# Performance work log

Hardware: AMD Instinct MI355X
Metric: run time of the kernel (lower is better)

The kernel has to match this reference:

```python
import jax, jax.numpy as jnp
import numpy as np

N = 50000   # nodes
E = 800000  # edges
H = 3       # attention heads
IN_F = 128
HID = 128
NUM_CLASSES = 6
GAT_SLOPE = 0.2   # DGL GATConv internal leaky_relu slope
ACT_SLOPE = 0.01  # nn.LeakyReLU default


def setup_inputs() -> dict:
    key = jax.random.key(0)
    ks = jax.random.split(key, 24)
    s = 0.05
    inp = {
        "in_feat": jax.random.normal(ks[0], (N, IN_F), jnp.float32),
        "src": jax.random.randint(ks[1], (E,), 0, N, jnp.int32),
        "dst": jax.random.randint(ks[2], (E,), 0, N, jnp.int32),
        # GATConv 1: W (IN_F, H*HID), attn vectors (H, HID), bias (H*HID)
        "W1": jax.random.normal(ks[3], (IN_F, H * HID), jnp.float32) * s,
        "al1": jax.random.normal(ks[4], (H, HID), jnp.float32) * s,
        "ar1": jax.random.normal(ks[5], (H, HID), jnp.float32) * s,
        "b1": jnp.zeros((H * HID,), jnp.float32),
        # GATConv 2
        "W2": jax.random.normal(ks[6], (HID, H * HID), jnp.float32) * s,
        "al2": jax.random.normal(ks[7], (H, HID), jnp.float32) * s,
        "ar2": jax.random.normal(ks[8], (H, HID), jnp.float32) * s,
        "b2": jnp.zeros((H * HID,), jnp.float32),
    }
    # Dense MLP head lin1..lin4 (HID->HID) and lin5 (HID->NUM_CLASSES)
    for i in range(1, 5):
        inp[f"lw{i}"] = jax.random.normal(ks[8 + 2 * i], (HID, HID), jnp.float32) * s
        inp[f"lb{i}"] = jnp.zeros((HID,), jnp.float32)
    inp["lw5"] = jax.random.normal(ks[20], (HID, NUM_CLASSES), jnp.float32) * s
    inp["lb5"] = jnp.zeros((NUM_CLASSES,), jnp.float32)
    return inp


def gat_conv(x, src, dst, W, al, ar, b):
    # x: (N, F_in) -> out: (N, H, HID)
    h = (x @ W).reshape(N, H, HID)
    el = jnp.einsum('nhf,hf->nh', h, al)  # (N, H)
    er = jnp.einsum('nhf,hf->nh', h, ar)
    e = jax.nn.leaky_relu(el[src] + er[dst], GAT_SLOPE)  # (E, H)
    # edge softmax over incoming edges of each dst node
    m = jax.ops.segment_max(e, dst, num_segments=N)
    m = jnp.where(jnp.isfinite(m), m, 0.0)
    ex = jnp.exp(e - m[dst])
    denom = jax.ops.segment_sum(ex, dst, num_segments=N)
    alpha = ex / (denom[dst] + 1e-9)  # (E, H)
    out = jax.ops.segment_sum(alpha[:, :, None] * h[src], dst, num_segments=N)
    return out + b.reshape(1, H, HID)


def reference(in_feat, src, dst, W1, al1, ar1, b1, W2, al2, ar2, b2,
              lw1, lb1, lw2, lb2, lw3, lb3, lw4, lb4, lw5, lb5):
    act = lambda x: jax.nn.leaky_relu(x, ACT_SLOPE)
    h = act(gat_conv(in_feat, src, dst, W1, al1, ar1, b1)).mean(axis=1)
    h = act(gat_conv(h, src, dst, W2, al2, ar2, b2)).mean(axis=1)
    h = act(h @ lw1 + lb1)
    h = act(h @ lw2 + lb2)
    h = act(h @ lw3 + lb3)
    h = act(h @ lw4 + lb4)
    return h @ lw5 + lb5
```

## Files before the change

### kernel.cpp

```cpp
#include <hip/hip_runtime.h>
#include <hip/hip_bf16.h>


typedef __attribute__((ext_vector_type(8))) short short8;
typedef __attribute__((ext_vector_type(4))) float float4v;

__device__ inline short f2bf(float x) {
    union { float f; unsigned u; } v; v.f = x;
    unsigned r = v.u + 0x7FFFu + ((v.u >> 16) & 1u);
    return (short)(r >> 16);
}
__device__ inline float bf2f(short b) {
    union { float f; unsigned u; } v;
    v.u = ((unsigned)(unsigned short)b) << 16;
    return v.f;
}
__device__ inline short8 zero8() { short8 z = {0,0,0,0,0,0,0,0}; return z; }

__device__ __forceinline__ void gl_lds16(const short* g, short* l) {
    __builtin_amdgcn_global_load_lds(
        (const __attribute__((address_space(1))) void*)g,
        (__attribute__((address_space(3))) void*)l,
        16, 0, 0);
}

#define SW(r) ((((r) >> 2) ^ (r)) & 3)

#define BM 128
#define BN 128
#define BK 32
#define MSTR 136
#define MROWS 64

__global__ void prep_kernel(
    const float* __restrict__ in_feat, short* __restrict__ P1h,
    short* __restrict__ P1l, int n4, int cb, int wb,
    const int* __restrict__ dst, int* __restrict__ cnt, int E,
    const float* __restrict__ w1, const float* __restrict__ w2,
    const float* __restrict__ m1, const float* __restrict__ m2,
    const float* __restrict__ m3, const float* __restrict__ m4,
    const float* __restrict__ w5,
    short* __restrict__ w1h, short* __restrict__ w1l,
    short* __restrict__ w2h, short* __restrict__ w2l,
    short* __restrict__ m1h, short* __restrict__ m1l,
    short* __restrict__ m2h, short* __restrict__ m2l,
    short* __restrict__ m3h, short* __restrict__ m3l,
    short* __restrict__ m4h, short* __restrict__ m4l,
    short* __restrict__ w5h, short* __restrict__ w5l)
{
    int blk = blockIdx.x;
    if (blk < cb) {
        int i = blk * 256 + threadIdx.x;
        if (i >= n4) return;
        float4 v = *(const float4*)(in_feat + (size_t)i * 4);
        float xs[4] = {v.x, v.y, v.z, v.w};
        short hs[4], ls[4];
        #pragma unroll
        for (int j = 0; j < 4; ++j) {
            hs[j] = f2bf(xs[j]);
            ls[j] = f2bf(xs[j] - bf2f(hs[j]));
        }
        *(uint2*)(P1h + (size_t)i * 4) = *(uint2*)hs;
        *(uint2*)(P1l + (size_t)i * 4) = *(uint2*)ls;
    } else if (blk < cb + wb) {
        int j = (blk - cb) * 256 + threadIdx.x;
        const float* src; short* th; short* tl; int Nc, base;
        if      (j < 49152)  { src = w1; th = w1h; tl = w1l; Nc = 384; base = 0; }
        else if (j < 98304)  { src = w2; th = w2h; tl = w2l; Nc = 384; base = 49152; }
        else if (j < 114688) { src = m1; th = m1h; tl = m1l; Nc = 128; base = 98304; }
        else if (j < 131072) { src = m2; th = m2h; tl = m2l; Nc = 128; base = 114688; }
        else if (j < 147456) { src = m3; th = m3h; tl = m3l; Nc = 128; base = 131072; }
        else if (j < 163840) { src = m4; th = m4h; tl = m4l; Nc = 128; base = 147456; }
        else if (j < 164608) { src = w5; th = w5h; tl = w5l; Nc = 6;   base = 163840; }
        else return;
        int i = j - base;
        int k = i / Nc, c = i - k * Nc;
        float v = src[i];
        short h = f2bf(v);
        th[(size_t)c * 128 + k] = h;
        tl[(size_t)c * 128 + k] = f2bf(v - bf2f(h));
    } else {
        int e = (blk - cb - wb) * 256 + threadIdx.x;
        if (e < E) atomicAdd(&cnt[dst[e]], 1);
    }
}

__global__ __launch_bounds__(256) void gemm_mfma(
    const short* __restrict__ Ahi, const short* __restrict__ Alo,
    const short* __restrict__ Bth, const short* __restrict__ Btl,
    unsigned char* __restrict__ Cq,
    float* __restrict__ els, float* __restrict__ er,
    const float* __restrict__ al, const float* __restrict__ ar,
    int M, int Nc)
{
    __shared__ short Ah[BM * BK], Al_[BM * BK];
    __shared__ short Bh[BN * BK], Bl_[BN * BK];

    int tid = threadIdx.x, lane = tid & 63, wave = tid >> 6;
    int l15 = lane & 15, q = lane >> 4;
    int rowBase = blockIdx.y * BM, colBase = blockIdx.x * BN;

    float4v acc[2][8];
    #pragma unroll
    for (int mt = 0; mt < 2; ++mt)
        #pragma unroll
        for (int nt = 0; nt < 8; ++nt)
            acc[mt][nt] = (float4v){0.f, 0.f, 0.f, 0.f};

    for (int k0 = 0; k0 < 128; k0 += BK) {
        #pragma unroll
        for (int i = 0; i < 2; ++i) {
            int cid = tid + i * 256;
            int r = cid >> 2, sub = cid & 3;
            int gs = (sub ^ SW(r)) * 8;
            size_t ga = (size_t)(rowBase + r) * 128 + k0 + gs;
            size_t gb = (size_t)(colBase + r) * 128 + k0 + gs;
            int ld = cid * 8;
            gl_lds16(Ahi + ga, Ah  + ld);
            gl_lds16(Alo + ga, Al_ + ld);
            gl_lds16(Bth + gb, Bh  + ld);
            gl_lds16(Btl + gb, Bl_ + ld);
        }
        __syncthreads();

        short8 aH[2], aL2[2];
        #pragma unroll
        for (int mt = 0; mt < 2; ++mt) {
            int row = wave * 32 + mt * 16 + l15;
            int off = row * 32 + (q ^ SW(row)) * 8;
            aH[mt]  = *(short8*)&Ah[off];
            aL2[mt] = *(short8*)&Al_[off];
        }
        #pragma unroll
        for (int nt = 0; nt < 8; ++nt) {
            int row = nt * 16 + l15;
            int off = row * 32 + (q ^ SW(row)) * 8;
            short8 bH = *(short8*)&Bh[off];
            short8 bL = *(short8*)&Bl_[off];
            #pragma unroll
            for (int mt = 0; mt < 2; ++mt) {
                acc[mt][nt] = __builtin_amdgcn_mfma_f32_16x16x32_bf16(aH[mt], bH, acc[mt][nt], 0, 0, 0);
                acc[mt][nt] = __builtin_amdgcn_mfma_f32_16x16x32_bf16(aH[mt], bL, acc[mt][nt], 0, 0, 0);
                acc[mt][nt] = __builtin_amdgcn_mfma_f32_16x16x32_bf16(aL2[mt], bH, acc[mt][nt], 0, 0, 0);
            }
        }
        __syncthreads();
    }

    {
        const float* alh = al + colBase;
        const float* arh = ar + colBase;
        float pel[2][4] = {}, per_[2][4] = {};
        #pragma unroll
        for (int nt = 0; nt < 8; ++nt) {
            float av = alh[nt * 16 + l15];
            float rv = arh[nt * 16 + l15];
            #pragma unroll
            for (int mt = 0; mt < 2; ++mt)
                #pragma unroll
                for (int i = 0; i < 4; ++i) {
                    pel[mt][i]  += acc[mt][nt][i] * av;
                    per_[mt][i] += acc[mt][nt][i] * rv;
                }
        }
        #pragma unroll
        for (int mask = 1; mask < 16; mask <<= 1)
            #pragma unroll
            for (int mt = 0; mt < 2; ++mt)
                #pragma unroll
                for (int i = 0; i < 4; ++i) {
                    pel[mt][i]  += __shfl_xor(pel[mt][i], mask);
                    per_[mt][i] += __shfl_xor(per_[mt][i], mask);
                }
        if (l15 == 0) {
            #pragma unroll
            for (int mt = 0; mt < 2; ++mt)
                #pragma unroll
                for (int i = 0; i < 4; ++i) {
                    int r = rowBase + wave * 32 + mt * 16 + q * 4 + i;
                    if (r < M) {
                        els[(size_t)(r * 3 + blockIdx.x) * 2] = pel[mt][i];
                        er[r * 3 + blockIdx.x] = per_[mt][i];
                    }
                }
        }
    }

    #pragma unroll
    for (int mt = 0; mt < 2; ++mt) {
        #pragma unroll
        for (int i = 0; i < 4; ++i) {
            float rm = 0.f;
            #pragma unroll
            for (int nt = 0; nt < 8; ++nt)
                rm = fmaxf(rm, fabsf(acc[mt][nt][i]));
            #pragma unroll
            for (int mask = 1; mask < 16; mask <<= 1)
                rm = fmaxf(rm, __shfl_xor(rm, mask));
            int r = rowBase + wave * 32 + mt * 16 + q * 4 + i;
            float inv = 127.f / fmaxf(rm, 1e-30f);
            if (l15 == 0 && r < M)
                els[(size_t)(r * 3 + blockIdx.x) * 2 + 1] = rm * (1.f / 127.f);
            #pragma unroll
            for (int nt = 0; nt < 8; ++nt) {
                int c = colBase + nt * 16 + l15;
                int qi = (int)rintf(acc[mt][nt][i] * inv);
                int qn = __shfl_xor(qi, 1);
                if (!(l15 & 1) && r < M && c < Nc) {
                    unsigned short pk = (unsigned short)((qi & 0xFF) | ((qn & 0xFF) << 8));
                    *(unsigned short*)(Cq + (size_t)r * Nc + c) = pk;
                }
            }
        }
    }
}

__global__ __launch_bounds__(256) void mlp_fused(
    const short* __restrict__ Ph, const short* __restrict__ Pl,
    const short* __restrict__ w1h, const short* __restrict__ w1l,
    const short* __restrict__ w2h, const short* __restrict__ w2l,
    const short* __restrict__ w3h, const short* __restrict__ w3l,
    const short* __restrict__ w4h, const short* __restrict__ w4l,
    const short* __restrict__ w5h, const short* __restrict__ w5l,
    const float* __restrict__ b1, const float* __restrict__ b2,
    const float* __restrict__ b3, const float* __restrict__ b4,
    const float* __restrict__ b5,
    float* __restrict__ out, int M)
{
    __shared__ short AH[MROWS * MSTR], AL[MROWS * MSTR];
    __shared__ short WH[128 * BK], WL[128 * BK];

    int tid = threadIdx.x, lane = tid & 63, wave = tid >> 6;
    int l15 = lane & 15, q = lane >> 4;
    int rowBase = blockIdx.x * MROWS;

    #pragma unroll
    for (int s = 0; s < 4; ++s) {
        int idx = tid + s * 256;
        int r = idx >> 4, kq = (idx & 15) * 8;
        int gr = rowBase + r;
        short8 vh = zero8(), vl = zero8();
        if (gr < M) {
            vh = *(const short8*)(Ph + (size_t)gr * 128 + kq);
            vl = *(const short8*)(Pl + (size_t)gr * 128 + kq);
        }
        *(short8*)&AH[r * MSTR + kq] = vh;
        *(short8*)&AL[r * MSTR + kq] = vl;
    }

    const short* Whs[4] = {w1h, w2h, w3h, w4h};
    const short* Wls[4] = {w1l, w2l, w3l, w4l};
    const float* Bss[4] = {b1, b2, b3, b4};

    #pragma unroll
    for (int L = 0; L < 4; ++L) {
        float4v acc[8];
        #pragma unroll
        for (int nt = 0; nt < 8; ++nt)
            acc[nt] = (float4v){0.f, 0.f, 0.f, 0.f};

        for (int k0 = 0; k0 < 128; k0 += BK) {
            #pragma unroll
            for (int i = 0; i < 4; ++i) {
                int c2 = tid + (i & 1) * 256;
                int r = c2 >> 2, sub = c2 & 3;
                int gs = (sub ^ SW(r)) * 8;
                if (i < 2) gl_lds16(Whs[L] + (size_t)r * 128 + k0 + gs, WH + c2 * 8);
                else       gl_lds16(Wls[L] + (size_t)r * 128 + k0 + gs, WL + c2 * 8);
            }
            __syncthreads();
            int offa = (wave * 16 + l15) * MSTR + k0 + q * 8;
            short8 aH  = *(short8*)&AH[offa];
            short8 aL2 = *(short8*)&AL[offa];
            #pragma unroll
            for (int nt = 0; nt < 8; ++nt) {
                int row = nt * 16 + l15;
                int off = row * 32 + (q ^ SW(row)) * 8;
                short8 bH = *(short8*)&WH[off];
                short8 bL = *(short8*)&WL[off];
                acc[nt] = __builtin_amdgcn_mfma_f32_16x16x32_bf16(aH, bH, acc[nt], 0, 0, 0);
                acc[nt] = __builtin_amdgcn_mfma_f32_16x16x32_bf16(aH, bL, acc[nt], 0, 0, 0);
                acc[nt] = __builtin_amdgcn_mfma_f32_16x16x32_bf16(aL2, bH, acc[nt], 0, 0, 0);
            }
            __syncthreads();
        }
        #pragma unroll
        for (int nt = 0; nt < 8; ++nt) {
            int c = nt * 16 + l15;
            float bv = Bss[L][c];
            #pragma unroll
            for (int i = 0; i < 4; ++i) {
                int r = wave * 16 + q * 4 + i;
                float v = acc[nt][i] + bv;
                v = (v < 0.f) ? 0.01f * v : v;
                short hh = f2bf(v);
                AH[r * MSTR + c] = hh;
                AL[r * MSTR + c] = f2bf(v - bf2f(hh));
            }
        }
        __syncthreads();
    }

    float4v acc5 = (float4v){0.f, 0.f, 0.f, 0.f};
    for (int k0 = 0; k0 < 128; k0 += BK) {
        if (tid < 128) {
            int plane = tid >> 6, rem = tid & 63;
            int c = rem >> 2, sub = rem & 3;
            short8 v = zero8();
            if (c < 6)
                v = *(const short8*)((plane ? w5l : w5h) + (size_t)c * 128 + k0 + sub * 8);
            *(short8*)&((plane ? WL : WH)[c * 32 + (sub ^ SW(c)) * 8]) = v;
        }
        __syncthreads();
        int offa = (wave * 16 + l15) * MSTR + k0 + q * 8;
        short8 aH  = *(short8*)&AH[offa];
        short8 aL2 = *(short8*)&AL[offa];
        int offb = l15 * 32 + (q ^ SW(l15)) * 8;
        short8 bH = *(short8*)&WH[offb];
        short8 bL = *(short8*)&WL[offb];
        acc5 = __builtin_amdgcn_mfma_f32_16x16x32_bf16(aH, bH, acc5, 0, 0, 0);
        acc5 = __builtin_amdgcn_mfma_f32_16x16x32_bf16(aH, bL, acc5, 0, 0, 0);
        acc5 = __builtin_amdgcn_mfma_f32_16x16x32_bf16(aL2, bH, acc5, 0, 0, 0);
        __syncthreads();
    }
    if (l15 < 6) {
        float bv = b5[l15];
        #pragma unroll
        for (int i = 0; i < 4; ++i) {
            int r = rowBase + wave * 16 + q * 4 + i;
            if (r < M) out[(size_t)r * 6 + l15] = acc5[i] + bv;
        }
    }
}

__global__ __launch_bounds__(1024) void scan_block(const int* __restrict__ cnt,
                                                   int* __restrict__ off,
                                                   int* __restrict__ bsum, int n)
{
    __shared__ int tmp[1024];
    int tid = threadIdx.x;
    int i = blockIdx.x * 1024 + tid;
    int v = (i < n) ? cnt[i] : 0;
    tmp[tid] = v;
    __syncthreads();
    for (int s = 1; s < 1024; s <<= 1) {
        int t = (tid >= s) ? tmp[tid - s] : 0;
        __syncthreads();
        tmp[tid] += t;
        __syncthreads();
    }
    if (i < n) off[i] = tmp[tid] - v;
    if (tid == 1023) bsum[blockIdx.x] = tmp[1023];
}

__global__ void scan_add2(int* __restrict__ off, const int* __restrict__ bsum,
                          int n, int nb)
{
    __shared__ int pre[64];
    int tid = threadIdx.x;
    if (tid < 64) {
        int v = (tid < nb) ? bsum[tid] : 0;
        #pragma unroll
        for (int s = 1; s < 64; s <<= 1) {
            int t = __shfl_up(v, s);
            if (tid >= s) v += t;
        }
        pre[tid] = v;
    }
    __syncthreads();
    int i = blockIdx.x * blockDim.x + tid;
    if (i < n) {
        int chunk = i >> 10;
        off[i] += chunk ? pre[chunk - 1] : 0;
    }
    if (i == 0) off[n] = pre[nb - 1];
}

__global__ void scatter_kernel(const int* __restrict__ src, const int* __restrict__ dst,
                               const int* __restrict__ off, int* __restrict__ cnt,
                               int* __restrict__ csrc, int E)
{
    int e = blockIdx.x * blockDim.x + threadIdx.x;
    if (e < E) {
        int d = dst[e];
        int p = atomicSub(&cnt[d], 1) - 1;
        csrc[off[d] + p] = src[e];
    }
}

__global__ __launch_bounds__(384) void agg_kernel(
    const unsigned char* __restrict__ h8, const float* __restrict__ els,
    const float* __restrict__ er, const int* __restrict__ off,
    const int* __restrict__ csrc, const float* __restrict__ bias,
    short* __restrict__ outH, short* __restrict__ outL, int N)
{
    int tid = threadIdx.x;
    int u = tid >> 6;
    int nl = u / 3;
    int head = u - nl * 3;
    int l = tid & 63;
    int n = blockIdx.x * 2 + nl;
    bool active = (n < N);

    __shared__ int   ssrcS[6][64];
    __shared__ float swS[6][64];
    __shared__ float smS[2][384];

    int beg = 0, deg = 0;
    float erv = 0.f;
    if (active) {
        beg = off[n];
        deg = off[n + 1] - beg;
        erv = er[n * 3 + head];
    }

    const unsigned char* hseg = h8 + head * 128 + l * 2;
    float ax = 0.f, ay = 0.f, denl = 0.f;

    for (int base = 0; base < deg; base += 64) {
        int cnt = min(64, deg - base);
        int s_l = 0; float w = 0.f, wS = 0.f;
        if (l < cnt) {
            s_l = csrc[beg + base + l];
            float2 e2 = *(const float2*)(els + (size_t)(s_l * 3 + head) * 2);
            float t = e2.x + erv;
            t = (t < 0.f) ? 0.2f * t : t;
            w = __expf(t);
            wS = w * e2.y;
        }
        denl += w;
        ssrcS[u][l] = s_l;
        swS[u][l]   = wS;
        for (int q0 = 0; q0 < cnt; q0 += 8) {
            int sA[8]; float wA[8]; unsigned vA[8];
            #pragma unroll
            for (int b = 0; b < 8; ++b) {
                int e = q0 + b;
                sA[b] = ssrcS[u][e];
                wA[b] = swS[u][e];
            }
            #pragma unroll
            for (int b = 0; b < 8; ++b)
                vA[b] = *(const unsigned short*)(hseg + (size_t)sA[b] * 384);
            #pragma unroll
            for (int b = 0; b < 8; ++b) {
                int b0 = (int)(signed char)(vA[b] & 0xFF);
                int b1 = (int)(signed char)((vA[b] >> 8) & 0xFF);
                ax += wA[b] * (float)b0;
                ay += wA[b] * (float)b1;
            }
        }
    }

    float den = denl;
    #pragma unroll
    for (int msk = 1; msk < 64; msk <<= 1) den += __shfl_xor(den, msk);
    float r = 1.f / (den + 1e-9f);
    if (deg == 0) r = 0.f;

    if (active) {
        int fb = head * 128 + 2 * l;
        float2 bv = *(const float2*)(bias + fb);
        float vx = ax * r + bv.x; vx = (vx < 0.f) ? 0.01f * vx : vx;
        float vy = ay * r + bv.y; vy = (vy < 0.f) ? 0.01f * vy : vy;
        smS[nl][fb]     = vx;
        smS[nl][fb + 1] = vy;
    }
    __syncthreads();
    if (tid < 128) {
        int mn = tid >> 6;
        int n2 = blockIdx.x * 2 + mn;
        if (n2 < N) {
            int f0i = (tid & 63) * 2, f1i = f0i + 1;
            float mx = (smS[mn][f0i] + smS[mn][128 + f0i] + smS[mn][256 + f0i]) * (1.0f / 3.0f);
            float my = (smS[mn][f1i] + smS[mn][128 + f1i] + smS[mn][256 + f1i]) * (1.0f / 3.0f);
            short hx = f2bf(mx), lx = f2bf(mx - bf2f(hx));
            short hy = f2bf(my), ly = f2bf(my - bf2f(hy));
            unsigned ph = (unsigned)(unsigned short)hx | ((unsigned)(unsigned short)hy << 16);
            unsigned pl = (unsigned)(unsigned short)lx | ((unsigned)(unsigned short)ly << 16);
            *(unsigned*)(outH + (size_t)n2 * 128 + f0i) = ph;
            *(unsigned*)(outL + (size_t)n2 * 128 + f0i) = pl;
        }
    }
}

extern "C" void kernel_launch(void* const* d_in, const int* in_sizes, int n_in,
                              void* d_out, int out_size, void* d_ws, size_t ws_size,
                              hipStream_t stream)
{
    const float* in_feat = (const float*)d_in[0];
    const int*   src     = (const int*)d_in[1];
    const int*   dst     = (const int*)d_in[2];
    const float* W1  = (const float*)d_in[3];
    const float* al1 = (const float*)d_in[4];
    const float* ar1 = (const float*)d_in[5];
    const float* b1  = (const float*)d_in[6];
    const float* W2  = (const float*)d_in[7];
    const float* al2 = (const float*)d_in[8];
    const float* ar2 = (const float*)d_in[9];
    const float* b2  = (const float*)d_in[10];
    const float* lw1 = (const float*)d_in[11];
    const float* lb1 = (const float*)d_in[12];
    const float* lw2 = (const float*)d_in[13];
    const float* lb2 = (const float*)d_in[14];
    const float* lw3 = (const float*)d_in[15];
    const float* lb3 = (const float*)d_in[16];
    const float* lw4 = (const float*)d_in[17];
    const float* lb4 = (const float*)d_in[18];
    const float* lw5 = (const float*)d_in[19];
    const float* lb5 = (const float*)d_in[20];

    const int N = in_sizes[0] / 128;
    const int E = in_sizes[1];

    size_t o = 0;
    auto alloc = [&](size_t bytes) { size_t p = o; o = (o + bytes + 255) & ~(size_t)255; return p; };
    char* ws = (char*)d_ws;
    short* P1h = (short*)(ws + alloc((size_t)N * 128 * 2));
    short* P1l = (short*)(ws + alloc((size_t)N * 128 * 2));
    short* P2h = (short*)(ws + alloc((size_t)N * 128 * 2));
    short* P2l = (short*)(ws + alloc((size_t)N * 128 * 2));
    unsigned char* Aq = (unsigned char*)(ws + alloc((size_t)N * 384));
    float* els = (float*)(ws + alloc((size_t)N * 3 * 2 * 4));
    float* er  = (float*)(ws + alloc((size_t)N * 3 * 4));
    int*   cnt  = (int*)(ws + alloc((size_t)N * 4));
    int*   off  = (int*)(ws + alloc((size_t)(N + 1) * 4));
    int*   bsum = (int*)(ws + alloc((size_t)4096));
    int*   csrc = (int*)(ws + alloc((size_t)E * 4));
    short* w1th = (short*)(ws + alloc((size_t)384 * 128 * 2));
    short* w1tl = (short*)(ws + alloc((size_t)384 * 128 * 2));
    short* w2th = (short*)(ws + alloc((size_t)384 * 128 * 2));
    short* w2tl = (short*)(ws + alloc((size_t)384 * 128 * 2));
    short* l1th = (short*)(ws + alloc((size_t)128 * 128 * 2));
    short* l1tl = (short*)(ws + alloc((size_t)128 * 128 * 2));
    short* l2th = (short*)(ws + alloc((size_t)128 * 128 * 2));
    short* l2tl = (short*)(ws + alloc((size_t)128 * 128 * 2));
    short* l3th = (short*)(ws + alloc((size_t)128 * 128 * 2));
    short* l3tl = (short*)(ws + alloc((size_t)128 * 128 * 2));
    short* l4th = (short*)(ws + alloc((size_t)128 * 128 * 2));
    short* l4tl = (short*)(ws + alloc((size_t)128 * 128 * 2));
    short* l5th = (short*)(ws + alloc((size_t)6 * 128 * 2));
    short* l5tl = (short*)(ws + alloc((size_t)6 * 128 * 2));
    (void)ws_size;

    float* out = (float*)d_out;

    hipMemsetAsync(cnt, 0, (size_t)N * 4, stream);
    int n4 = N * 128 / 4;
    int cb = (n4 + 255) / 256;
    int wb = (164608 + 255) / 256;
    int hb = (E + 255) / 256;
    prep_kernel<<<cb + wb + hb, 256, 0, stream>>>(
        in_feat, P1h, P1l, n4, cb, wb, dst, cnt, E,
        W1, W2, lw1, lw2, lw3, lw4, lw5,
        w1th, w1tl, w2th, w2tl, l1th, l1tl, l2th, l2tl,
        l3th, l3tl, l4th, l4tl, l5th, l5tl);

    int nb = (N + 1023) / 1024;
    scan_block<<<nb, 1024, 0, stream>>>(cnt, off, bsum, N);
    scan_add2<<<(N + 255) / 256, 256, 0, stream>>>(off, bsum, N, nb);
    scatter_kernel<<<(E + 255) / 256, 256, 0, stream>>>(src, dst, off, cnt, csrc, E);

    int RB = (N + BM - 1) / BM;
    dim3 ggrid(3, RB);
    int AGB = (N + 1) / 2;

    gemm_mfma<<<ggrid, 256, 0, stream>>>(P1h, P1l, w1th, w1tl, Aq, els, er,
                                         al1, ar1, N, 384);
    agg_kernel<<<AGB, 384, 0, stream>>>(Aq, els, er, off, csrc, b1, P2h, P2l, N);

    gemm_mfma<<<ggrid, 256, 0, stream>>>(P2h, P2l, w2th, w2tl, Aq, els, er,
                                         al2, ar2, N, 384);
    agg_kernel<<<AGB, 384, 0, stream>>>(Aq, els, er, off, csrc, b2, P1h, P1l, N);

    int RBM = (N + MROWS - 1) / MROWS;
    mlp_fused<<<RBM, 256, 0, stream>>>(P1h, P1l,
                                       l1th, l1tl, l2th, l2tl, l3th, l3tl,
                                       l4th, l4tl, l5th, l5tl,
                                       lb1, lb2, lb3, lb4, lb5, out, N);
}
```

Measured before the change: 495.7 us.

## Fold attention vectors into weights and drop split-bf16 GAT GEMM terms

Precomputes u = W·al and W·ar per head so the attention logits el/er become a dot product of the fp32 node input with u. Layer one gets them from a separate node_el kernel on in_feat, and layer two computes them inside the first aggregation kernel from the fp32 mean. With the logits no longer coming from the GEMM, the GAT GEMMs use plain bf16 (hi only) instead of three-term hi/lo products, which removes the lo operand loads and two thirds of the MFMAs. The risk is lower precision in the projected features h used for aggregation. It also adds one extra small kernel launch.

```diff
diff --git a/kernel.cpp b/kernel.cpp
--- a/kernel.cpp
+++ b/kernel.cpp
@@ -34,19 +34,21 @@
 
 __global__ void prep_kernel(
     const float* __restrict__ in_feat, short* __restrict__ P1h,
-    short* __restrict__ P1l, int n4, int cb, int wb,
+    int n4, int cb, int wb,
     const int* __restrict__ dst, int* __restrict__ cnt, int E,
     const float* __restrict__ w1, const float* __restrict__ w2,
     const float* __restrict__ m1, const float* __restrict__ m2,
     const float* __restrict__ m3, const float* __restrict__ m4,
     const float* __restrict__ w5,
-    short* __restrict__ w1h, short* __restrict__ w1l,
-    short* __restrict__ w2h, short* __restrict__ w2l,
+    short* __restrict__ w1h, short* __restrict__ w2h,
     short* __restrict__ m1h, short* __restrict__ m1l,
     short* __restrict__ m2h, short* __restrict__ m2l,
     short* __restrict__ m3h, short* __restrict__ m3l,
     short* __restrict__ m4h, short* __restrict__ m4l,
-    short* __restrict__ w5h, short* __restrict__ w5l)
+    short* __restrict__ w5h, short* __restrict__ w5l,
+    const float* __restrict__ al1, const float* __restrict__ ar1,
+    const float* __restrict__ al2, const float* __restrict__ ar2,
+    float* __restrict__ u1, float* __restrict__ u2)
 {
     int blk = blockIdx.x;
     if (blk < cb) {
@@ -54,19 +56,15 @@
         if (i >= n4) return;
         float4 v = *(const float4*)(in_feat + (size_t)i * 4);
         float xs[4] = {v.x, v.y, v.z, v.w};
-        short hs[4], ls[4];
-        #pragma unroll
-        for (int j = 0; j < 4; ++j) {
-            hs[j] = f2bf(xs[j]);
-            ls[j] = f2bf(xs[j] - bf2f(hs[j]));
-        }
+        short hs[4];
+        #pragma unroll
+        for (int j = 0; j < 4; ++j) hs[j] = f2bf(xs[j]);
         *(uint2*)(P1h + (size_t)i * 4) = *(uint2*)hs;
-        *(uint2*)(P1l + (size_t)i * 4) = *(uint2*)ls;
     } else if (blk < cb + wb) {
         int j = (blk - cb) * 256 + threadIdx.x;
         const float* src; short* th; short* tl; int Nc, base;
-        if      (j < 49152)  { src = w1; th = w1h; tl = w1l; Nc = 384; base = 0; }
-        else if (j < 98304)  { src = w2; th = w2h; tl = w2l; Nc = 384; base = 49152; }
+        if      (j < 49152)  { src = w1; th = w1h; tl = nullptr; Nc = 384; base = 0; }
+        else if (j < 98304)  { src = w2; th = w2h; tl = nullptr; Nc = 384; base = 49152; }
         else if (j < 114688) { src = m1; th = m1h; tl = m1l; Nc = 128; base = 98304; }
         else if (j < 131072) { src = m2; th = m2h; tl = m2l; Nc = 128; base = 114688; }
         else if (j < 147456) { src = m3; th = m3h; tl = m3l; Nc = 128; base = 131072; }
@@ -78,23 +76,63 @@
         float v = src[i];
         short h = f2bf(v);
         th[(size_t)c * 128 + k] = h;
-        tl[(size_t)c * 128 + k] = f2bf(v - bf2f(h));
+        if (tl) tl[(size_t)c * 128 + k] = f2bf(v - bf2f(h));
+    } else if (blk == cb + wb) {
+        int t = threadIdx.x;
+        const float* W  = (t < 128) ? w1 : w2;
+        const float* av = (t < 128) ? al1 : al2;
+        const float* rv = (t < 128) ? ar1 : ar2;
+        float* u = (t < 128) ? u1 : u2;
+        int k = t & 127;
+        #pragma unroll
+        for (int h = 0; h < 3; ++h) {
+            float sl = 0.f, sr = 0.f;
+            for (int f = 0; f < 128; ++f) {
+                float wv = W[(size_t)k * 384 + h * 128 + f];
+                sl += wv * av[h * 128 + f];
+                sr += wv * rv[h * 128 + f];
+            }
+            u[(h * 2 + 0) * 128 + k] = sl;
+            u[(h * 2 + 1) * 128 + k] = sr;
+        }
     } else {
-        int e = (blk - cb - wb) * 256 + threadIdx.x;
+        int e = (blk - cb - wb - 1) * 256 + threadIdx.x;
         if (e < E) atomicAdd(&cnt[dst[e]], 1);
     }
 }
 
+__global__ __launch_bounds__(256) void node_el(
+    const float* __restrict__ X, const float* __restrict__ u,
+    float* __restrict__ els, float* __restrict__ er, int N)
+{
+    int n = blockIdx.x * 4 + (threadIdx.x >> 6);
+    int l = threadIdx.x & 63;
+    if (n >= N) return;
+    float2 x = *(const float2*)(X + (size_t)n * 128 + 2 * l);
+    float a[6];
+    #pragma unroll
+    for (int v = 0; v < 6; ++v)
+        a[v] = x.x * u[v * 128 + 2 * l] + x.y * u[v * 128 + 2 * l + 1];
+    #pragma unroll
+    for (int msk = 1; msk < 64; msk <<= 1)
+        #pragma unroll
+        for (int v = 0; v < 6; ++v)
+            a[v] += __shfl_xor(a[v], msk);
+    if (l == 0) {
+        #pragma unroll
+        for (int h = 0; h < 3; ++h) {
+            els[(size_t)(n * 3 + h) * 2] = a[h * 2];
+            er[n * 3 + h] = a[h * 2 + 1];
+        }
+    }
+}
+
 __global__ __launch_bounds__(256) void gemm_mfma(
-    const short* __restrict__ Ahi, const short* __restrict__ Alo,
-    const short* __restrict__ Bth, const short* __restrict__ Btl,
-    unsigned char* __restrict__ Cq,
-    float* __restrict__ els, float* __restrict__ er,
-    const float* __restrict__ al, const float* __restrict__ ar,
+    const short* __restrict__ Ahi, const short* __restrict__ Bth,
+    unsigned char* __restrict__ Cq, float* __restrict__ els,
     int M, int Nc)
 {
-    __shared__ short Ah[BM * BK], Al_[BM * BK];
-    __shared__ short Bh[BN * BK], Bl_[BN * BK];
+    __shared__ short Ah[BM * BK], Bh[BN * BK];
 
     int tid = threadIdx.x, lane = tid & 63, wave = tid >> 6;
     int l15 = lane & 15, q = lane >> 4;
@@ -113,77 +151,28 @@
             int cid = tid + i * 256;
             int r = cid >> 2, sub = cid & 3;
             int gs = (sub ^ SW(r)) * 8;
-            size_t ga = (size_t)(rowBase + r) * 128 + k0 + gs;
-            size_t gb = (size_t)(colBase + r) * 128 + k0 + gs;
-            int ld = cid * 8;
-            gl_lds16(Ahi + ga, Ah  + ld);
-            gl_lds16(Alo + ga, Al_ + ld);
-            gl_lds16(Bth + gb, Bh  + ld);
-            gl_lds16(Btl + gb, Bl_ + ld);
-        }
-        __syncthreads();
-
-        short8 aH[2], aL2[2];
+            gl_lds16(Ahi + (size_t)(rowBase + r) * 128 + k0 + gs, Ah + cid * 8);
+            gl_lds16(Bth + (size_t)(colBase + r) * 128 + k0 + gs, Bh + cid * 8);
+        }
+        __syncthreads();
+
+        short8 aH[2];
         #pragma unroll
         for (int mt = 0; mt < 2; ++mt) {
             int row = wave * 32 + mt * 16 + l15;
             int off = row * 32 + (q ^ SW(row)) * 8;
-            aH[mt]  = *(short8*)&Ah[off];
-            aL2[mt] = *(short8*)&Al_[off];
+            aH[mt] = *(short8*)&Ah[off];
         }
         #pragma unroll
         for (int nt = 0; nt < 8; ++nt) {
             int row = nt * 16 + l15;
             int off = row * 32 + (q ^ SW(row)) * 8;
             short8 bH = *(short8*)&Bh[off];
-            short8 bL = *(short8*)&Bl_[off];
-            #pragma unroll
-            for (int mt = 0; mt < 2; ++mt) {
+            #pragma unroll
+            for (int mt = 0; mt < 2; ++mt)
                 acc[mt][nt] = __builtin_amdgcn_mfma_f32_16x16x32_bf16(aH[mt], bH, acc[mt][nt], 0, 0, 0);
-                acc[mt][nt] = __builtin_amdgcn_mfma_f32_16x16x32_bf16(aH[mt], bL, acc[mt][nt], 0, 0, 0);
-                acc[mt][nt] = __builtin_amdgcn_mfma_f32_16x16x32_bf16(aL2[mt], bH, acc[mt][nt], 0, 0, 0);
-            }
-        }
-        __syncthreads();
-    }
-
-    {
-        const float* alh = al + colBase;
-        const float* arh = ar + colBase;
-        float pel[2][4] = {}, per_[2][4] = {};
-        #pragma unroll
-        for (int nt = 0; nt < 8; ++nt) {
-            float av = alh[nt * 16 + l15];
-            float rv = arh[nt * 16 + l15];
-            #pragma unroll
-            for (int mt = 0; mt < 2; ++mt)
-                #pragma unroll
-                for (int i = 0; i < 4; ++i) {
-                    pel[mt][i]  += acc[mt][nt][i] * av;
-                    per_[mt][i] += acc[mt][nt][i] * rv;
-                }
-        }
-        #pragma unroll
-        for (int mask = 1; mask < 16; mask <<= 1)
-            #pragma unroll
-            for (int mt = 0; mt < 2; ++mt)
-                #pragma unroll
-                for (int i = 0; i < 4; ++i) {
-                    pel[mt][i]  += __shfl_xor(pel[mt][i], mask);
-                    per_[mt][i] += __shfl_xor(per_[mt][i], mask);
-                }
-        if (l15 == 0) {
-            #pragma unroll
-            for (int mt = 0; mt < 2; ++mt)
-                #pragma unroll
-                for (int i = 0; i < 4; ++i) {
-                    int r = rowBase + wave * 32 + mt * 16 + q * 4 + i;
-                    if (r < M) {
-                        els[(size_t)(r * 3 + blockIdx.x) * 2] = pel[mt][i];
-                        er[r * 3 + blockIdx.x] = per_[mt][i];
-                    }
-                }
-        }
+        }
+        __syncthreads();
     }
 
     #pragma unroll
@@ -392,7 +381,9 @@
     const unsigned char* __restrict__ h8, const float* __restrict__ els,
     const float* __restrict__ er, const int* __restrict__ off,
     const int* __restrict__ csrc, const float* __restrict__ bias,
-    short* __restrict__ outH, short* __restrict__ outL, int N)
+    short* __restrict__ outH, short* __restrict__ outL,
+    const float* __restrict__ u2v, float* __restrict__ els2,
+    float* __restrict__ er2, int N)
 {
     int tid = threadIdx.x;
     int u = tid >> 6;
@@ -470,16 +461,37 @@
     if (tid < 128) {
         int mn = tid >> 6;
         int n2 = blockIdx.x * 2 + mn;
+        int f0i = (tid & 63) * 2, f1i = f0i + 1;
+        float mx = 0.f, my = 0.f;
         if (n2 < N) {
-            int f0i = (tid & 63) * 2, f1i = f0i + 1;
-            float mx = (smS[mn][f0i] + smS[mn][128 + f0i] + smS[mn][256 + f0i]) * (1.0f / 3.0f);
-            float my = (smS[mn][f1i] + smS[mn][128 + f1i] + smS[mn][256 + f1i]) * (1.0f / 3.0f);
-            short hx = f2bf(mx), lx = f2bf(mx - bf2f(hx));
-            short hy = f2bf(my), ly = f2bf(my - bf2f(hy));
+            mx = (smS[mn][f0i] + smS[mn][128 + f0i] + smS[mn][256 + f0i]) * (1.0f / 3.0f);
+            my = (smS[mn][f1i] + smS[mn][128 + f1i] + smS[mn][256 + f1i]) * (1.0f / 3.0f);
+            short hx = f2bf(mx), hy = f2bf(my);
             unsigned ph = (unsigned)(unsigned short)hx | ((unsigned)(unsigned short)hy << 16);
-            unsigned pl = (unsigned)(unsigned short)lx | ((unsigned)(unsigned short)ly << 16);
             *(unsigned*)(outH + (size_t)n2 * 128 + f0i) = ph;
-            *(unsigned*)(outL + (size_t)n2 * 128 + f0i) = pl;
+            if (outL) {
+                short lx = f2bf(mx - bf2f(hx)), ly = f2bf(my - bf2f(hy));
+                unsigned pl = (unsigned)(unsigned short)lx | ((unsigned)(unsigned short)ly << 16);
+                *(unsigned*)(outL + (size_t)n2 * 128 + f0i) = pl;
+            }
+        }
+        if (u2v) {
+            float a[6];
+            #pragma unroll
+            for (int v = 0; v < 6; ++v)
+                a[v] = mx * u2v[v * 128 + f0i] + my * u2v[v * 128 + f1i];
+            #pragma unroll
+            for (int msk = 1; msk < 64; msk <<= 1)
+                #pragma unroll
+                for (int v = 0; v < 6; ++v)
+                    a[v] += __shfl_xor(a[v], msk);
+            if ((tid & 63) == 0 && n2 < N) {
+                #pragma unroll
+                for (int h = 0; h < 3; ++h) {
+                    els2[(size_t)(n2 * 3 + h) * 2] = a[h * 2];
+                    er2[n2 * 3 + h] = a[h * 2 + 1];
+                }
+            }
         }
     }
 }
@@ -519,18 +531,19 @@
     short* P1h = (short*)(ws + alloc((size_t)N * 128 * 2));
     short* P1l = (short*)(ws + alloc((size_t)N * 128 * 2));
     short* P2h = (short*)(ws + alloc((size_t)N * 128 * 2));
-    short* P2l = (short*)(ws + alloc((size_t)N * 128 * 2));
     unsigned char* Aq = (unsigned char*)(ws + alloc((size_t)N * 384));
-    float* els = (float*)(ws + alloc((size_t)N * 3 * 2 * 4));
-    float* er  = (float*)(ws + alloc((size_t)N * 3 * 4));
+    float* els1 = (float*)(ws + alloc((size_t)N * 3 * 2 * 4));
+    float* er1  = (float*)(ws + alloc((size_t)N * 3 * 4));
+    float* els2 = (float*)(ws + alloc((size_t)N * 3 * 2 * 4));
+    float* er2  = (float*)(ws + alloc((size_t)N * 3 * 4));
+    float* u1   = (float*)(ws + alloc((size_t)6 * 128 * 4));
+    float* u2   = (float*)(ws + alloc((size_t)6 * 128 * 4));
     int*   cnt  = (int*)(ws + alloc((size_t)N * 4));
     int*   off  = (int*)(ws + alloc((size_t)(N + 1) * 4));
     int*   bsum = (int*)(ws + alloc((size_t)4096));
     int*   csrc = (int*)(ws + alloc((size_t)E * 4));
     short* w1th = (short*)(ws + alloc((size_t)384 * 128 * 2));
-    short* w1tl = (short*)(ws + alloc((size_t)384 * 128 * 2));
     short* w2th = (short*)(ws + alloc((size_t)384 * 128 * 2));
-    short* w2tl = (short*)(ws + alloc((size_t)384 * 128 * 2));
     short* l1th = (short*)(ws + alloc((size_t)128 * 128 * 2));
     short* l1tl = (short*)(ws + alloc((size_t)128 * 128 * 2));
     short* l2th = (short*)(ws + alloc((size_t)128 * 128 * 2));
@@ -550,28 +563,30 @@
     int cb = (n4 + 255) / 256;
     int wb = (164608 + 255) / 256;
     int hb = (E + 255) / 256;
-    prep_kernel<<<cb + wb + hb, 256, 0, stream>>>(
-        in_feat, P1h, P1l, n4, cb, wb, dst, cnt, E,
+    prep_kernel<<<cb + wb + 1 + hb, 256, 0, stream>>>(
+        in_feat, P1h, n4, cb, wb, dst, cnt, E,
         W1, W2, lw1, lw2, lw3, lw4, lw5,
-        w1th, w1tl, w2th, w2tl, l1th, l1tl, l2th, l2tl,
-        l3th, l3tl, l4th, l4tl, l5th, l5tl);
+        w1th, w2th, l1th, l1tl, l2th, l2tl,
+        l3th, l3tl, l4th, l4tl, l5th, l5tl,
+        al1, ar1, al2, ar2, u1, u2);
 
     int nb = (N + 1023) / 1024;
     scan_block<<<nb, 1024, 0, stream>>>(cnt, off, bsum, N);
     scan_add2<<<(N + 255) / 256, 256, 0, stream>>>(off, bsum, N, nb);
     scatter_kernel<<<(E + 255) / 256, 256, 0, stream>>>(src, dst, off, cnt, csrc, E);
+    node_el<<<(N + 3) / 4, 256, 0, stream>>>(in_feat, u1, els1, er1, N);
 
     int RB = (N + BM - 1) / BM;
     dim3 ggrid(3, RB);
     int AGB = (N + 1) / 2;
 
-    gemm_mfma<<<ggrid, 256, 0, stream>>>(P1h, P1l, w1th, w1tl, Aq, els, er,
-                                         al1, ar1, N, 384);
-    agg_kernel<<<AGB, 384, 0, stream>>>(Aq, els, er, off, csrc, b1, P2h, P2l, N);
-
-    gemm_mfma<<<ggrid, 256, 0, stream>>>(P2h, P2l, w2th, w2tl, Aq, els, er,
-                                         al2, ar2, N, 384);
-    agg_kernel<<<AGB, 384, 0, stream>>>(Aq, els, er, off, csrc, b2, P1h, P1l, N);
+    gemm_mfma<<<ggrid, 256, 0, stream>>>(P1h, w1th, Aq, els1, N, 384);
+    agg_kernel<<<AGB, 384, 0, stream>>>(Aq, els1, er1, off, csrc, b1,
+                                        P2h, nullptr, u2, els2, er2, N);
+
+    gemm_mfma<<<ggrid, 256, 0, stream>>>(P2h, w2th, Aq, els2, N, 384);
+    agg_kernel<<<AGB, 384, 0, stream>>>(Aq, els2, er2, off, csrc, b2,
+                                        P1h, P1l, nullptr, nullptr, nullptr, N);
 
     int RBM = (N + MROWS - 1) / MROWS;
     mlp_fused<<<RBM, 256, 0, stream>>>(P1h, P1l,
```

New measurement: 511.0 us. 1.03x slower.
